# Kernel optimization log

Measured on AMD Instinct MI355X. Metric: run time of the kernel, lower is better.

Reference implementation:

```python
import jax, jax.numpy as jnp
import numpy as np
import itertools

N_LEVELS = 16
F = 2
OFFSETS = [0, 4096, 12096, 27721, 60489, 124489, 249489, 511633, 1023633,
           1547921, 2072209, 2596497, 3120785, 3645073, 4169361, 4693649, 5217937]
RESOLUTIONS = [16, 20, 25, 32, 40, 50, 64, 80, 101, 128, 161, 203, 256, 322, 406, 512]
# Instant-NGP spatial hash primes (first prime = 1)
PRIMES = np.array([1, 2654435761, 805459861], dtype=np.uint32)
CORNERS = np.array(list(itertools.product([0, 1], repeat=3)), dtype=np.int32)  # (8,3)
B = 1 << 20


def setup_inputs() -> dict:
    key = jax.random.key(0)
    k1, k2 = jax.random.split(key)
    xyz = jax.random.uniform(k1, (B, 3), dtype=jnp.float32)  # points in [0,1)
    embeddings = jax.random.normal(k2, (OFFSETS[-1], F), dtype=jnp.float32) * 0.01
    return {
        'xyz': xyz,
        'embeddings': embeddings,
        'min_xyz': jnp.zeros((3,), jnp.float32),
        'max_xyz': jnp.ones((3,), jnp.float32),
    }


def _hashgrid_encode(xyz, embeddings, min_xyz, max_xyz):
    # normalize to [0,1] inside the grid bbox
    xyz_n = (xyz - min_xyz) / (max_xyz - min_xyz)  # (B,3)
    corners_u = jnp.asarray(CORNERS).astype(jnp.uint32)          # (8,3)
    corners_f = jnp.asarray(CORNERS).astype(jnp.float32)         # (8,3)
    primes = jnp.asarray(PRIMES)                                  # (3,) uint32
    outs = []
    for l in range(N_LEVELS):
        res = RESOLUTIONS[l]
        size = OFFSETS[l + 1] - OFFSETS[l]
        pos = xyz_n * (res - 1)                                   # (B,3) in [0,res-1]
        pos0 = jnp.clip(jnp.floor(pos), 0.0, res - 2)             # lower corner
        w = pos - pos0                                            # (B,3) trilinear frac
        p0 = pos0.astype(jnp.uint32)
        idx3 = p0[:, None, :] + corners_u[None]                   # (B,8,3)
        if res ** 3 <= size:
            # dense level: linear index
            idx = idx3[..., 0] * jnp.uint32(res * res) + idx3[..., 1] * jnp.uint32(res) + idx3[..., 2]
        else:
            # hashed level: xor of prime-multiplied coords (uint32 wraparound)
            idx = (idx3[..., 0] * primes[0]) ^ (idx3[..., 1] * primes[1]) ^ (idx3[..., 2] * primes[2])
            idx = idx % jnp.uint32(size)
        idx = idx.astype(jnp.int32) + OFFSETS[l]                  # (B,8) global entry id
        # trilinear weights: prod_d [ c_d ? w_d : 1-w_d ]
        wc = jnp.prod(corners_f[None] * w[:, None, :] + (1.0 - corners_f[None]) * (1.0 - w[:, None, :]), axis=-1)  # (B,8)
        feats = embeddings[idx]                                   # (B,8,F) gather
        outs.append(jnp.einsum('bc,bcf->bf', wc, feats))          # (B,F)
    return jnp.concatenate(outs, axis=-1)                         # (B, L*F)


def reference(xyz, embeddings, min_xyz, max_xyz):
    return _hashgrid_encode(xyz, embeddings, min_xyz, max_xyz)
```

## Files before the change

### kernel.cpp

```cpp
#include <hip/hip_runtime.h>
#include <stdint.h>


#define NLEV 16

__global__ __launch_bounds__(256, 4) void hashgrid_fwd(
    const float* __restrict__ xyz,
    const float2* __restrict__ emb,
    const float* __restrict__ mn,
    const float* __restrict__ mx,
    float* __restrict__ out,
    int npts)
{
    constexpr int RES[16] = {16,20,25,32,40,50,64,80,101,128,161,203,256,322,406,512};
    constexpr uint32_t OFFS[17] = {0u,4096u,12096u,27721u,60489u,124489u,249489u,511633u,
                                   1023633u,1547921u,2072209u,2596497u,3120785u,3645073u,
                                   4169361u,4693649u,5217937u};
    constexpr uint32_t P1 = 2654435761u, P2 = 805459861u;

    const int b = blockIdx.x * blockDim.x + threadIdx.x;
    if (b >= npts) return;

    const float mn0 = mn[0], mn1 = mn[1], mn2 = mn[2];
    const float inv0 = 1.0f / (mx[0] - mn0);
    const float inv1 = 1.0f / (mx[1] - mn1);
    const float inv2 = 1.0f / (mx[2] - mn2);

    const float xn = (xyz[3*b+0] - mn0) * inv0;
    const float yn = (xyz[3*b+1] - mn1) * inv1;
    const float zn = (xyz[3*b+2] - mn2) * inv2;

    float o[32];

#pragma unroll
    for (int l = 0; l < NLEV; ++l) {
        const int res = RES[l];
        const uint32_t off = OFFS[l];
        const uint32_t size = OFFS[l+1] - OFFS[l];
        const float scale = (float)(res - 1);
        const float hi = (float)(res - 2);

        const float px = xn * scale, py = yn * scale, pz = zn * scale;
        const float fx = fminf(fmaxf(floorf(px), 0.0f), hi);
        const float fy = fminf(fmaxf(floorf(py), 0.0f), hi);
        const float fz = fminf(fmaxf(floorf(pz), 0.0f), hi);
        const float wx1 = px - fx, wy1 = py - fy, wz1 = pz - fz;
        const float wx0 = 1.0f - wx1, wy0 = 1.0f - wy1, wz0 = 1.0f - wz1;
        const uint32_t ix = (uint32_t)fx, iy = (uint32_t)fy, iz = (uint32_t)fz;

        float ax = 0.0f, ay = 0.0f;

        const bool dense = ((long long)res * res * res) <= (long long)size;
        if (dense) {
            const uint32_t dx = (uint32_t)(res * res);
            const uint32_t dy = (uint32_t)res;
            const uint32_t base = off + ix * dx + iy * dy + iz;
            {
                float2 e0 = emb[base];           float2 e1 = emb[base + 1];
                float wxy = wx0 * wy0;
                ax += wxy * (wz0 * e0.x + wz1 * e1.x);
                ay += wxy * (wz0 * e0.y + wz1 * e1.y);
            }
            {
                float2 e0 = emb[base + dy];      float2 e1 = emb[base + dy + 1];
                float wxy = wx0 * wy1;
                ax += wxy * (wz0 * e0.x + wz1 * e1.x);
                ay += wxy * (wz0 * e0.y + wz1 * e1.y);
            }
            {
                float2 e0 = emb[base + dx];      float2 e1 = emb[base + dx + 1];
                float wxy = wx1 * wy0;
                ax += wxy * (wz0 * e0.x + wz1 * e1.x);
                ay += wxy * (wz0 * e0.y + wz1 * e1.y);
            }
            {
                float2 e0 = emb[base + dx + dy]; float2 e1 = emb[base + dx + dy + 1];
                float wxy = wx1 * wy1;
                ax += wxy * (wz0 * e0.x + wz1 * e1.x);
                ay += wxy * (wz0 * e0.y + wz1 * e1.y);
            }
        } else {
            const uint32_t hx0 = ix,      hx1 = ix + 1u;
            const uint32_t hy0 = iy * P1, hy1 = hy0 + P1;
            const uint32_t hz0 = iz * P2, hz1 = hz0 + P2;
            const uint32_t i000 = ((hx0 ^ hy0 ^ hz0) % size) + off;
            const uint32_t i001 = ((hx0 ^ hy0 ^ hz1) % size) + off;
            const uint32_t i010 = ((hx0 ^ hy1 ^ hz0) % size) + off;
            const uint32_t i011 = ((hx0 ^ hy1 ^ hz1) % size) + off;
            const uint32_t i100 = ((hx1 ^ hy0 ^ hz0) % size) + off;
            const uint32_t i101 = ((hx1 ^ hy0 ^ hz1) % size) + off;
            const uint32_t i110 = ((hx1 ^ hy1 ^ hz0) % size) + off;
            const uint32_t i111 = ((hx1 ^ hy1 ^ hz1) % size) + off;
            float2 e;
            float w;
            e = emb[i000]; w = wx0*wy0*wz0; ax += w*e.x; ay += w*e.y;
            e = emb[i001]; w = wx0*wy0*wz1; ax += w*e.x; ay += w*e.y;
            e = emb[i010]; w = wx0*wy1*wz0; ax += w*e.x; ay += w*e.y;
            e = emb[i011]; w = wx0*wy1*wz1; ax += w*e.x; ay += w*e.y;
            e = emb[i100]; w = wx1*wy0*wz0; ax += w*e.x; ay += w*e.y;
            e = emb[i101]; w = wx1*wy0*wz1; ax += w*e.x; ay += w*e.y;
            e = emb[i110]; w = wx1*wy1*wz0; ax += w*e.x; ay += w*e.y;
            e = emb[i111]; w = wx1*wy1*wz1; ax += w*e.x; ay += w*e.y;
        }
        o[2*l]   = ax;
        o[2*l+1] = ay;
    }

    float4* ov = (float4*)(out + (size_t)b * 32);
#pragma unroll
    for (int i = 0; i < 8; ++i)
        ov[i] = make_float4(o[4*i+0], o[4*i+1], o[4*i+2], o[4*i+3]);
}

extern "C" void kernel_launch(void* const* d_in, const int* in_sizes, int n_in,
                              void* d_out, int out_size, void* d_ws, size_t ws_size,
                              hipStream_t stream) {
    const float*  xyz = (const float*)d_in[0];
    const float2* emb = (const float2*)d_in[1];
    const float*  mn  = (const float*)d_in[2];
    const float*  mx  = (const float*)d_in[3];
    float* out = (float*)d_out;

    const int npts = in_sizes[0] / 3;
    const int block = 256;
    const int grid = (npts + block - 1) / block;

    hipLaunchKernelGGL(hashgrid_fwd, dim3(grid), dim3(block), 0, stream,
                       xyz, emb, mn, mx, out, npts);
}
```

Baseline: 788.9 us.

## Split hashgrid levels across grid y-dimension with phase-per-level hashed blocks

Launches a 2D grid where y=0 computes the eight dense levels per point and y=1..8 each compute one hashed level, so each block touches only one hash table slice at a time. The aim is better cache locality in the embedding gathers and more parallelism and occupancy (launch bounds raised to 8 waves). The modulo by table size is replaced with a power-of-two mask, which is exact because every hashed level has size 524288. In exchange, xyz is reloaded and normalised nine times per point, and the output is written as scattered float2 stores instead of full-row float4 stores.

```diff
diff --git a/kernel.cpp b/kernel.cpp
--- a/kernel.cpp
+++ b/kernel.cpp
@@ -2,9 +2,9 @@
 #include <stdint.h>
 
 
-#define NLEV 16
+__device__ __constant__ int kRES[16] = {16,20,25,32,40,50,64,80,101,128,161,203,256,322,406,512};
 
-__global__ __launch_bounds__(256, 4) void hashgrid_fwd(
+__global__ __launch_bounds__(256, 8) void hashgrid_phased(
     const float* __restrict__ xyz,
     const float2* __restrict__ emb,
     const float* __restrict__ mn,
@@ -12,11 +12,9 @@
     float* __restrict__ out,
     int npts)
 {
-    constexpr int RES[16] = {16,20,25,32,40,50,64,80,101,128,161,203,256,322,406,512};
-    constexpr uint32_t OFFS[17] = {0u,4096u,12096u,27721u,60489u,124489u,249489u,511633u,
-                                   1023633u,1547921u,2072209u,2596497u,3120785u,3645073u,
-                                   4169361u,4693649u,5217937u};
     constexpr uint32_t P1 = 2654435761u, P2 = 805459861u;
+    constexpr uint32_t HASH_MASK = 0x7FFFFu;
+    constexpr uint32_t HASH_BASE = 1023633u;
 
     const int b = blockIdx.x * blockDim.x + threadIdx.x;
     if (b >= npts) return;
@@ -30,31 +28,32 @@
     const float yn = (xyz[3*b+1] - mn1) * inv1;
     const float zn = (xyz[3*b+2] - mn2) * inv2;
 
-    float o[32];
+    const int y = blockIdx.y;
 
+    if (y == 0) {
+        constexpr int RES[8] = {16,20,25,32,40,50,64,80};
+        constexpr uint32_t OFFS[8] = {0u,4096u,12096u,27721u,60489u,124489u,249489u,511633u};
+        float o[16];
 #pragma unroll
-    for (int l = 0; l < NLEV; ++l) {
-        const int res = RES[l];
-        const uint32_t off = OFFS[l];
-        const uint32_t size = OFFS[l+1] - OFFS[l];
-        const float scale = (float)(res - 1);
-        const float hi = (float)(res - 2);
+        for (int l = 0; l < 8; ++l) {
+            const int res = RES[l];
+            const uint32_t off = OFFS[l];
+            const float scale = (float)(res - 1);
+            const float hi = (float)(res - 2);
 
-        const float px = xn * scale, py = yn * scale, pz = zn * scale;
-        const float fx = fminf(fmaxf(floorf(px), 0.0f), hi);
-        const float fy = fminf(fmaxf(floorf(py), 0.0f), hi);
-        const float fz = fminf(fmaxf(floorf(pz), 0.0f), hi);
-        const float wx1 = px - fx, wy1 = py - fy, wz1 = pz - fz;
-        const float wx0 = 1.0f - wx1, wy0 = 1.0f - wy1, wz0 = 1.0f - wz1;
-        const uint32_t ix = (uint32_t)fx, iy = (uint32_t)fy, iz = (uint32_t)fz;
+            const float px = xn * scale, py = yn * scale, pz = zn * scale;
+            const float fx = fminf(fmaxf(floorf(px), 0.0f), hi);
+            const float fy = fminf(fmaxf(floorf(py), 0.0f), hi);
+            const float fz = fminf(fmaxf(floorf(pz), 0.0f), hi);
+            const float wx1 = px - fx, wy1 = py - fy, wz1 = pz - fz;
+            const float wx0 = 1.0f - wx1, wy0 = 1.0f - wy1, wz0 = 1.0f - wz1;
+            const uint32_t ix = (uint32_t)fx, iy = (uint32_t)fy, iz = (uint32_t)fz;
 
-        float ax = 0.0f, ay = 0.0f;
-
-        const bool dense = ((long long)res * res * res) <= (long long)size;
-        if (dense) {
             const uint32_t dx = (uint32_t)(res * res);
             const uint32_t dy = (uint32_t)res;
             const uint32_t base = off + ix * dx + iy * dy + iz;
+
+            float ax = 0.0f, ay = 0.0f;
             {
                 float2 e0 = emb[base];           float2 e1 = emb[base + 1];
                 float wxy = wx0 * wy0;
@@ -79,37 +78,58 @@
                 ax += wxy * (wz0 * e0.x + wz1 * e1.x);
                 ay += wxy * (wz0 * e0.y + wz1 * e1.y);
             }
-        } else {
-            const uint32_t hx0 = ix,      hx1 = ix + 1u;
-            const uint32_t hy0 = iy * P1, hy1 = hy0 + P1;
-            const uint32_t hz0 = iz * P2, hz1 = hz0 + P2;
-            const uint32_t i000 = ((hx0 ^ hy0 ^ hz0) % size) + off;
-            const uint32_t i001 = ((hx0 ^ hy0 ^ hz1) % size) + off;
-            const uint32_t i010 = ((hx0 ^ hy1 ^ hz0) % size) + off;
-            const uint32_t i011 = ((hx0 ^ hy1 ^ hz1) % size) + off;
-            const uint32_t i100 = ((hx1 ^ hy0 ^ hz0) % size) + off;
-            const uint32_t i101 = ((hx1 ^ hy0 ^ hz1) % size) + off;
-            const uint32_t i110 = ((hx1 ^ hy1 ^ hz0) % size) + off;
-            const uint32_t i111 = ((hx1 ^ hy1 ^ hz1) % size) + off;
-            float2 e;
-            float w;
-            e = emb[i000]; w = wx0*wy0*wz0; ax += w*e.x; ay += w*e.y;
-            e = emb[i001]; w = wx0*wy0*wz1; ax += w*e.x; ay += w*e.y;
-            e = emb[i010]; w = wx0*wy1*wz0; ax += w*e.x; ay += w*e.y;
-            e = emb[i011]; w = wx0*wy1*wz1; ax += w*e.x; ay += w*e.y;
-            e = emb[i100]; w = wx1*wy0*wz0; ax += w*e.x; ay += w*e.y;
-            e = emb[i101]; w = wx1*wy0*wz1; ax += w*e.x; ay += w*e.y;
-            e = emb[i110]; w = wx1*wy1*wz0; ax += w*e.x; ay += w*e.y;
-            e = emb[i111]; w = wx1*wy1*wz1; ax += w*e.x; ay += w*e.y;
+            o[2*l]   = ax;
+            o[2*l+1] = ay;
         }
-        o[2*l]   = ax;
-        o[2*l+1] = ay;
+        float4* ov = (float4*)(out + (size_t)b * 32);
+#pragma unroll
+        for (int i = 0; i < 4; ++i)
+            ov[i] = make_float4(o[4*i+0], o[4*i+1], o[4*i+2], o[4*i+3]);
+    } else {
+        const int l = y + 7;
+        const int res = kRES[l];
+        const uint32_t off = HASH_BASE + (uint32_t)(l - 8) * 524288u;
+
+        const float scale = (float)(res - 1);
+        const float hi = (float)(res - 2);
+
+        const float px = xn * scale, py = yn * scale, pz = zn * scale;
+        const float fx = fminf(fmaxf(floorf(px), 0.0f), hi);
+        const float fy = fminf(fmaxf(floorf(py), 0.0f), hi);
+        const float fz = fminf(fmaxf(floorf(pz), 0.0f), hi);
+        const float wx1 = px - fx, wy1 = py - fy, wz1 = pz - fz;
+        const float wx0 = 1.0f - wx1, wy0 = 1.0f - wy1, wz0 = 1.0f - wz1;
+        const uint32_t ix = (uint32_t)fx, iy = (uint32_t)fy, iz = (uint32_t)fz;
+
+        const uint32_t hx0 = ix,      hx1 = ix + 1u;
+        const uint32_t hy0 = iy * P1, hy1 = hy0 + P1;
+        const uint32_t hz0 = iz * P2, hz1 = hz0 + P2;
+
+        const uint32_t i000 = ((hx0 ^ hy0 ^ hz0) & HASH_MASK) + off;
+        const uint32_t i001 = ((hx0 ^ hy0 ^ hz1) & HASH_MASK) + off;
+        const uint32_t i010 = ((hx0 ^ hy1 ^ hz0) & HASH_MASK) + off;
+        const uint32_t i011 = ((hx0 ^ hy1 ^ hz1) & HASH_MASK) + off;
+        const uint32_t i100 = ((hx1 ^ hy0 ^ hz0) & HASH_MASK) + off;
+        const uint32_t i101 = ((hx1 ^ hy0 ^ hz1) & HASH_MASK) + off;
+        const uint32_t i110 = ((hx1 ^ hy1 ^ hz0) & HASH_MASK) + off;
+        const uint32_t i111 = ((hx1 ^ hy1 ^ hz1) & HASH_MASK) + off;
+
+        float2 e000 = emb[i000], e001 = emb[i001], e010 = emb[i010], e011 = emb[i011];
+        float2 e100 = emb[i100], e101 = emb[i101], e110 = emb[i110], e111 = emb[i111];
+
+        float ax, ay, w;
+        w = wx0*wy0*wz0; ax  = w*e000.x; ay  = w*e000.y;
+        w = wx0*wy0*wz1; ax += w*e001.x; ay += w*e001.y;
+        w = wx0*wy1*wz0; ax += w*e010.x; ay += w*e010.y;
+        w = wx0*wy1*wz1; ax += w*e011.x; ay += w*e011.y;
+        w = wx1*wy0*wz0; ax += w*e100.x; ay += w*e100.y;
+        w = wx1*wy0*wz1; ax += w*e101.x; ay += w*e101.y;
+        w = wx1*wy1*wz0; ax += w*e110.x; ay += w*e110.y;
+        w = wx1*wy1*wz1; ax += w*e111.x; ay += w*e111.y;
+
+        float2* op = (float2*)(out + (size_t)b * 32 + 2 * l);
+        *op = make_float2(ax, ay);
     }
-
-    float4* ov = (float4*)(out + (size_t)b * 32);
-#pragma unroll
-    for (int i = 0; i < 8; ++i)
-        ov[i] = make_float4(o[4*i+0], o[4*i+1], o[4*i+2], o[4*i+3]);
 }
 
 extern "C" void kernel_launch(void* const* d_in, const int* in_sizes, int n_in,
@@ -123,8 +143,8 @@
 
     const int npts = in_sizes[0] / 3;
     const int block = 256;
-    const int grid = (npts + block - 1) / block;
+    const int grid_x = (npts + block - 1) / block;
 
-    hipLaunchKernelGGL(hashgrid_fwd, dim3(grid), dim3(block), 0, stream,
+    hipLaunchKernelGGL(hashgrid_phased, dim3(grid_x, 9), dim3(block), 0, stream,
                        xyz, emb, mn, mx, out, npts);
 }
```

New measurement: 778.7 us. Within noise of the previous version (-1.3%).
